# Kernel tuning notes

Measured on AMD Instinct MI355X. Metric: run time of the kernel, lower is better.

Reference implementation:

```python
import jax, jax.numpy as jnp
import numpy as np

B, T, D, H = 2, 2048, 1024, 16
Dh = D // H
SIG_SCALE = 1.0


def setup_inputs() -> dict:
    key = jax.random.key(0)
    ks = jax.random.split(key, 6)
    s = 1.0 / np.sqrt(D)
    return {
        "x": jax.random.normal(ks[0], (B, T, D), jnp.float32),
        "Wq": jax.random.normal(ks[1], (D, D), jnp.float32) * s,
        "Wk": jax.random.normal(ks[2], (D, D), jnp.float32) * s,
        "Wv": jax.random.normal(ks[3], (D, D), jnp.float32) * s,
        "Wb": jax.random.normal(ks[4], (D, H), jnp.float32) * s,
        "o_gamma": jnp.ones((H, Dh), jnp.float32),
        "Wo": jax.random.normal(ks[5], (D, D), jnp.float32) * s,
        "ln_g": jnp.ones((D,), jnp.float32),
        "ln_b": jnp.zeros((D,), jnp.float32),
    }


def _l2norm(a):
    return a * jax.lax.rsqrt(jnp.sum(a * a, -1, keepdims=True) + 1e-6)


def _deltanet(x, Wq, Wk, Wv, Wb, o_gamma, Wo):
    # bf16 projections (Block casts input to bfloat16), fp32 recurrence
    xb = x.astype(jnp.bfloat16)
    q = (xb @ Wq.astype(jnp.bfloat16)).astype(jnp.float32).reshape(B, T, H, Dh)
    k = (xb @ Wk.astype(jnp.bfloat16)).astype(jnp.float32).reshape(B, T, H, Dh)
    v = (xb @ Wv.astype(jnp.bfloat16)).astype(jnp.float32).reshape(B, T, H, Dh)
    q = _l2norm(jax.nn.silu(q))
    k = _l2norm(jax.nn.silu(k))
    # beta in [0, 2]: allows negative eigenvalues of (I - beta k k^T)
    beta = 2.0 * SIG_SCALE * jax.nn.sigmoid(
        (xb @ Wb.astype(jnp.bfloat16)).astype(jnp.float32))  # (B,T,H)

    def tohead(a):  # (B,T,H,Dh) -> (B*H, T, Dh)
        return a.transpose(0, 2, 1, 3).reshape(B * H, T, Dh)

    qh, kh, vh = tohead(q), tohead(k), tohead(v)
    bh = beta.transpose(0, 2, 1).reshape(B * H, T)

    def scan_one(qs, ks, vs, bs):
        def step(S, inp):
            k_t, v_t, q_t, b_t = inp
            # delta rule: S <- S + beta * (v - S k) k^T
            S = S + b_t * jnp.outer(v_t - S @ k_t, k_t)
            return S, S @ q_t
        _, o = jax.lax.scan(step, jnp.zeros((Dh, Dh), jnp.float32),
                            (ks, vs, qs, bs))
        return o  # (T, Dh)

    o = jax.vmap(scan_one)(qh, kh, vh, bh)  # (B*H, T, Dh)
    o = o.reshape(B, H, T, Dh).transpose(0, 2, 1, 3)  # (B,T,H,Dh)
    # per-head RMSNorm then output projection
    o = o * jax.lax.rsqrt(jnp.mean(o * o, -1, keepdims=True) + 1e-6) * o_gamma
    o = (o.reshape(B, T, D).astype(jnp.bfloat16) @ Wo.astype(jnp.bfloat16))
    return o.astype(jnp.float32)


def reference(x, Wq, Wk, Wv, Wb, o_gamma, Wo, ln_g, ln_b):
    y = _deltanet(x, Wq, Wk, Wv, Wb, o_gamma, Wo) + x  # residual in fp32
    mu = jnp.mean(y, -1, keepdims=True)
    var = jnp.mean(jnp.square(y - mu), -1, keepdims=True)
    y = (y - mu) * jax.lax.rsqrt(var + 1e-5) * ln_g + ln_b
    return y  # dropout is identity at inference; v_first passthrough is None
```

## Files before the change

### kernel.cpp

```cpp
#include <hip/hip_runtime.h>
#include <hip/hip_bf16.h>
#include <cstdint>

#define BB 2
#define TT 2048
#define DD 1024
#define HH 16
#define DH 64
#define MM (BB*TT)
constexpr int KDIM = 1024;
constexpr int NDIM = 1024;

typedef __bf16 bf16;
typedef __attribute__((ext_vector_type(8))) __bf16 bf16x8;
typedef __attribute__((ext_vector_type(4))) float f32x4;

#define MFMA(a,b,c) __builtin_amdgcn_mfma_f32_16x16x32_bf16((a),(b),(c),0,0,0)

__global__ __launch_bounds__(256) void k_cvt(const float* __restrict__ in, bf16* __restrict__ outp) {
    size_t i = ((size_t)blockIdx.x * 256 + threadIdx.x) * 8;
    float4 a = *(const float4*)(in + i);
    float4 b = *(const float4*)(in + i + 4);
    bf16x8 r;
    r[0] = (bf16)a.x; r[1] = (bf16)a.y; r[2] = (bf16)a.z; r[3] = (bf16)a.w;
    r[4] = (bf16)b.x; r[5] = (bf16)b.y; r[6] = (bf16)b.z; r[7] = (bf16)b.w;
    *(bf16x8*)(outp + i) = r;
}

__global__ __launch_bounds__(256) void k_transpose_cvt(const float* __restrict__ in, bf16* __restrict__ outp) {
    __shared__ float tile[64][65];
    const int tx = threadIdx.x & 63;
    const int ty = threadIdx.x >> 6;
    const int r0 = blockIdx.y * 64, c0 = blockIdx.x * 64;
#pragma unroll
    for (int i = 0; i < 16; ++i) {
        int rr = ty * 16 + i;
        tile[rr][tx] = in[(size_t)(r0 + rr) * 1024 + c0 + tx];
    }
    __syncthreads();
#pragma unroll
    for (int i = 0; i < 16; ++i) {
        int rr = ty * 16 + i;
        outp[(size_t)(c0 + rr) * 1024 + r0 + tx] = (bf16)tile[tx][rr];
    }
}

#define BM 128
#define BN 128
#define BKT 64

__device__ __forceinline__ void gemm_core(const bf16* __restrict__ A, const bf16* __restrict__ Bt,
                                          float* __restrict__ Cc) {
    __shared__ __align__(16) bf16 As[BM * BKT];
    __shared__ __align__(16) bf16 Bs[BN * BKT];
    const int tid  = threadIdx.x;
    const int lane = tid & 63;
    const int w    = tid >> 6;
    const int wr   = w >> 1, wc = w & 1;
    const int bm   = blockIdx.x * BM;
    const int bn   = blockIdx.y * BN;

    f32x4 acc[4][4];
#pragma unroll
    for (int m_ = 0; m_ < 4; ++m_)
#pragma unroll
        for (int n = 0; n < 4; ++n) acc[m_][n] = (f32x4){0.f, 0.f, 0.f, 0.f};

    const int srow = tid >> 3;
    const int sc   = tid & 7;
    const int sp   = sc ^ (srow & 7);
    const int fr   = lane & 15;
    const int fg   = lane >> 4;

    const bf16* Ap = A  + (size_t)(bm + srow) * KDIM + sc * 8;
    const bf16* Bp = Bt + (size_t)(bn + srow) * KDIM + sc * 8;

    for (int kt = 0; kt < KDIM; kt += BKT) {
        bf16x8 ar[4], br[4];
#pragma unroll
        for (int i = 0; i < 4; ++i) {
            ar[i] = *(const bf16x8*)(Ap + (size_t)i * 32 * KDIM + kt);
            br[i] = *(const bf16x8*)(Bp + (size_t)i * 32 * KDIM + kt);
        }
// ... 123 lines not shown
        if (t + 1 < TT) {
            const float* kn = kp + (size_t)(t + 1) * DD;
            const float* qn = qp + (size_t)(t + 1) * DD;
            nk0 = *(const float4*)(kn + 0);  nk1 = *(const float4*)(kn + 4);
            nk2 = *(const float4*)(kn + 8);  nk3 = *(const float4*)(kn + 12);
            nq0 = *(const float4*)(qn + 0);  nq1 = *(const float4*)(qn + 4);
            nq2 = *(const float4*)(qn + 8);  nq3 = *(const float4*)(qn + 12);
            nvv = vp[(size_t)(t + 1) * DD];
            nbt = bp[(size_t)(t + 1) * HH];
        }
        float a0, a1, a2, a3;
        a0 = S[0] * k0.x;  a1 = S[1] * k0.y;  a2 = S[2] * k0.z;  a3 = S[3] * k0.w;
        a0 = fmaf(S[4],  k1.x, a0); a1 = fmaf(S[5],  k1.y, a1); a2 = fmaf(S[6],  k1.z, a2); a3 = fmaf(S[7],  k1.w, a3);
        a0 = fmaf(S[8],  k2.x, a0); a1 = fmaf(S[9],  k2.y, a1); a2 = fmaf(S[10], k2.z, a2); a3 = fmaf(S[11], k2.w, a3);
        a0 = fmaf(S[12], k3.x, a0); a1 = fmaf(S[13], k3.y, a1); a2 = fmaf(S[14], k3.z, a2); a3 = fmaf(S[15], k3.w, a3);
        float sk = (a0 + a1) + (a2 + a3);
        sk += __shfl_xor(sk, 1); sk += __shfl_xor(sk, 2);
        const float wgt = bt * (vv - sk);
        float o0, o1, o2, o3;
        S[0]  = fmaf(wgt, k0.x, S[0]);  o0 = S[0] * q0.x;
        S[1]  = fmaf(wgt, k0.y, S[1]);  o1 = S[1] * q0.y;
        S[2]  = fmaf(wgt, k0.z, S[2]);  o2 = S[2] * q0.z;
        S[3]  = fmaf(wgt, k0.w, S[3]);  o3 = S[3] * q0.w;
        S[4]  = fmaf(wgt, k1.x, S[4]);  o0 = fmaf(S[4],  q1.x, o0);
        S[5]  = fmaf(wgt, k1.y, S[5]);  o1 = fmaf(S[5],  q1.y, o1);
        S[6]  = fmaf(wgt, k1.z, S[6]);  o2 = fmaf(S[6],  q1.z, o2);
        S[7]  = fmaf(wgt, k1.w, S[7]);  o3 = fmaf(S[7],  q1.w, o3);
        S[8]  = fmaf(wgt, k2.x, S[8]);  o0 = fmaf(S[8],  q2.x, o0);
        S[9]  = fmaf(wgt, k2.y, S[9]);  o1 = fmaf(S[9],  q2.y, o1);
        S[10] = fmaf(wgt, k2.z, S[10]); o2 = fmaf(S[10], q2.z, o2);
        S[11] = fmaf(wgt, k2.w, S[11]); o3 = fmaf(S[11], q2.w, o3);
        S[12] = fmaf(wgt, k3.x, S[12]); o0 = fmaf(S[12], q3.x, o0);
        S[13] = fmaf(wgt, k3.y, S[13]); o1 = fmaf(S[13], q3.y, o1);
        S[14] = fmaf(wgt, k3.z, S[14]); o2 = fmaf(S[14], q3.z, o2);
        S[15] = fmaf(wgt, k3.w, S[15]); o3 = fmaf(S[15], q3.w, o3);
        float oo = (o0 + o1) + (o2 + o3);
        oo += __shfl_xor(oo, 1); oo += __shfl_xor(oo, 2);
        if (seg == 0) op[(size_t)t * DD] = oo;
        k0 = nk0; k1 = nk1; k2 = nk2; k3 = nk3;
        q0 = nq0; q1 = nq1; q2 = nq2; q3 = nq3;
        vv = nvv; bt = nbt;
    }
}


__device__ __forceinline__ int uv_idx(int t, int vv) {
    return (((t >> 4) * 4 + (vv >> 4)) * 64 + (((t >> 2) & 3) * 16 + (vv & 15))) * 4 + (t & 3);
}

__global__ __launch_bounds__(256, 3) void k_prep(
        const float* __restrict__ q, const float* __restrict__ k, const float* __restrict__ v,
        const float* __restrict__ beta,
        bf16* __restrict__ L_out, bf16* __restrict__ nUk_h, bf16* __restrict__ nUk_l,
        bf16* __restrict__ Kt_h, bf16* __restrict__ Kt_l, float* __restrict__ Uv_out) {
    __shared__ float Ash[64][65];
    __shared__ bf16 Khi[64][72], Klo[64][72];
    __shared__ float bsh[64];

    const int tid = threadIdx.x;
    const int c = blockIdx.x, bh = blockIdx.y, b = bh >> 4, h = bh & 15;
    const int row0 = b * TT + c * 64, col0 = h * 64;
    const size_t off = ((size_t)bh * 32 + c) * 4096;
    const int lane = tid & 63, w = tid >> 6;
    const int fr = lane & 15, fg = lane >> 4;

    const int cslice = (w & 1) * 32;
    const float* rp = ((w >= 2) ? k : v) + (size_t)(row0 + lane) * DD + col0 + cslice;
    float4 rv[8];
#pragma unroll
    for (int a = 0; a < 8; ++a) rv[a] = *(const float4*)(rp + a * 4);
    const float* qfp = q + (size_t)(row0 + w * 16 + fr) * DD + col0 + fg * 8;
    float4 qa = *(const float4*)qfp, qb = *(const float4*)(qfp + 4);
    float4 qc = *(const float4*)(qfp + 32), qd = *(const float4*)(qfp + 36);
    const int tr = tid >> 2, cs = (tid & 3) * 16;
    float4 kv[4];
    const size_t rb = (size_t)(row0 + tr) * DD + col0 + cs;
#pragma unroll
    for (int j = 0; j < 4; ++j) kv[j] = *(const float4*)(k + rb + j * 4);

    if (tid < 64) bsh[tid] = beta[(size_t)(row0 + tid) * HH + h];
#pragma unroll
    for (int j = 0; j < 4; ++j) {
        int cb = cs + j * 4;
        float a0 = kv[j].x, a1 = kv[j].y, a2 = kv[j].z, a3 = kv[j].w;
        bf16 h0 = (bf16)a0, h1 = (bf16)a1, h2 = (bf16)a2, h3 = (bf16)a3;
        Khi[tr][cb] = h0; Khi[tr][cb+1] = h1; Khi[tr][cb+2] = h2; Khi[tr][cb+3] = h3;
        Klo[tr][cb]   = (bf16)(a0 - (float)h0);
        Klo[tr][cb+1] = (bf16)(a1 - (float)h1);
        Klo[tr][cb+2] = (bf16)(a2 - (float)h2);
        Klo[tr][cb+3] = (bf16)(a3 - (float)h3);
    }
    __syncthreads();

    {
        bf16x8 aqh0, aqh1;
        aqh0[0]=(bf16)qa.x; aqh0[1]=(bf16)qa.y; aqh0[2]=(bf16)qa.z; aqh0[3]=(bf16)qa.w;
        aqh0[4]=(bf16)qb.x; aqh0[5]=(bf16)qb.y; aqh0[6]=(bf16)qb.z; aqh0[7]=(bf16)qb.w;
        aqh1[0]=(bf16)qc.x; aqh1[1]=(bf16)qc.y; aqh1[2]=(bf16)qc.z; aqh1[3]=(bf16)qc.w;
        aqh1[4]=(bf16)qd.x; aqh1[5]=(bf16)qd.y; aqh1[6]=(bf16)qd.z; aqh1[7]=(bf16)qd.w;
        f32x4 accA[4], accL[4];
#pragma unroll
        for (int it = 0; it < 4; ++it) { accA[it] = (f32x4){0,0,0,0}; accL[it] = (f32x4){0,0,0,0}; }
        bf16x8 akh0 = *(const bf16x8*)&Khi[w*16+fr][fg*8];
        bf16x8 akh1 = *(const bf16x8*)&Khi[w*16+fr][fg*8+32];
        bf16x8 akl0 = *(const bf16x8*)&Klo[w*16+fr][fg*8];
        bf16x8 akl1 = *(const bf16x8*)&Klo[w*16+fr][fg*8+32];
#pragma unroll
        for (int it = 0; it < 4; ++it) {
            bf16x8 bh0 = *(const bf16x8*)&Khi[it*16+fr][fg*8];
            bf16x8 bl0 = *(const bf16x8*)&Klo[it*16+fr][fg*8];
            accA[it] = MFMA(akh0, bh0, accA[it]);
            accA[it] = MFMA(akh0, bl0, accA[it]);
            accA[it] = MFMA(akl0, bh0, accA[it]);
            accL[it] = MFMA(aqh0, bh0, accL[it]);
            bf16x8 bh1 = *(const bf16x8*)&Khi[it*16+fr][fg*8+32];
            bf16x8 bl1 = *(const bf16x8*)&Klo[it*16+fr][fg*8+32];
            accA[it] = MFMA(akh1, bh1, accA[it]);
            accA[it] = MFMA(akh1, bl1, accA[it]);
            accA[it] = MFMA(akl1, bh1, accA[it]);
            accL[it] = MFMA(aqh1, bh1, accL[it]);
        }
#pragma unroll
        for (int it = 0; it < 4; ++it)
#pragma unroll
            for (int j = 0; j < 4; ++j) {
                int tg = w * 16 + fg * 4 + j, ig = it * 16 + fr;
                Ash[tg][ig] = (ig < tg) ? bsh[tg] * accA[it][j] : 0.f;
                L_out[off + tg * 64 + ig] = (ig <= tg) ? (bf16)accL[it][j] : (bf16)0.f;
            }
    }
    __syncthreads();

    float bt = bsh[lane];
    float X[32];
#pragma unroll
    for (int a = 0; a < 8; ++a) {
        X[a*4+0] = bt * rv[a].x; X[a*4+1] = bt * rv[a].y;
        X[a*4+2] = bt * rv[a].z; X[a*4+3] = bt * rv[a].w;
    }
#pragma unroll 1
    for (int i = 0; i < 63; ++i) {
        float a = Ash[lane][i];
#pragma unroll
        for (int j = 0; j < 32; ++j) {
            float s = __uint_as_float(__builtin_amdgcn_readlane(__float_as_uint(X[j]), i));
            X[j] = fmaf(-a, s, X[j]);
        }
    }

    if (w < 2) {
#pragma unroll
        for (int j = 0; j < 32; ++j)
            Uv_out[off + uv_idx(lane, cslice + j)] = X[j];
    } else {
#pragma unroll
        for (int g = 0; g < 4; ++g) {
            bf16x8 hi8, lo8;
#pragma unroll
            for (int e = 0; e < 8; ++e) {
                float nk = -X[g*8+e];
                bf16 nh = (bf16)nk;
                hi8[e] = nh;
                lo8[e] = (bf16)(nk - (float)nh);
            }
            *(bf16x8*)(nUk_h + off + (size_t)lane*64 + cslice + g*8) = hi8;
            *(bf16x8*)(nUk_l + off + (size_t)lane*64 + cslice + g*8) = lo8;
        }
    }
#pragma unroll
    for (int j = 0; j < 16; ++j) {
        int vc = cs + j;
        Kt_h[off + (size_t)tr*64 + vc] = Khi[vc][tr];
        Kt_l[off + (size_t)tr*64 + vc] = Klo[vc][tr];
    }
}

struct Frag {
    bf16x8 nkh0, nkh1, nkl0, nkl1;
    bf16x8 kth0, kth1, ktl0, ktl1;
    bf16x8 lf0, lf1;
    float4 qa, qb, qc, qd;
    f32x4 uv0, uv1, uv2, uv3;
};

__device__ __forceinline__ void load_frags(Frag& F,
        const bf16* __restrict__ nUk_h, const bf16* __restrict__ nUk_l,
        const bf16* __restrict__ Kt_h, const bf16* __restrict__ Kt_l,
        const bf16* __restrict__ L_in, const float* __restrict__ Uv_in,
        const float* __restrict__ q, size_t off, size_t qbase, int w, int lane) {
    const int fr = lane & 15, fg = lane >> 4;
    const size_t ra = off + (size_t)(w * 16 + fr) * 64 + fg * 8;
    F.nkh0 = *(const bf16x8*)(nUk_h + ra); F.nkh1 = *(const bf16x8*)(nUk_h + ra + 32);
    F.nkl0 = *(const bf16x8*)(nUk_l + ra); F.nkl1 = *(const bf16x8*)(nUk_l + ra + 32);
    F.kth0 = *(const bf16x8*)(Kt_h + ra);  F.kth1 = *(const bf16x8*)(Kt_h + ra + 32);
    F.ktl0 = *(const bf16x8*)(Kt_l + ra);  F.ktl1 = *(const bf16x8*)(Kt_l + ra + 32);
    F.lf0  = *(const bf16x8*)(L_in + ra);  F.lf1  = *(const bf16x8*)(L_in + ra + 32);
    const float* qp = q + qbase + (size_t)(w * 16 + fr) * DD + fg * 8;
    F.qa = *(const float4*)qp;        F.qb = *(const float4*)(qp + 4);
    F.qc = *(const float4*)(qp + 32); F.qd = *(const float4*)(qp + 36);
    const float* up = Uv_in + off + w * 1024 + lane * 4;
    F.uv0 = *(const f32x4*)up;         F.uv1 = *(const f32x4*)(up + 256);
    F.uv2 = *(const f32x4*)(up + 512); F.uv3 = *(const f32x4*)(up + 768);
}

__device__ __forceinline__ void compute_chunk(const Frag& F, f32x4 (&Sacc)[4],
        float* __restrict__ o, int row0c, int col0, int w, int lane,
        bf16 (*ShT_h)[72], bf16 (*ShT_l)[72], bf16 (*Ut_h)[72], bf16 (*Ut_l)[72]) {
    const int fr = lane & 15, fg = lane >> 4;
    f32x4 Uacc[4] = {F.uv0, F.uv1, F.uv2, F.uv3};
#pragma unroll
    for (int vt = 0; vt < 4; ++vt) {
        const bf16* sh0 = &ShT_h[vt * 16 + fr][fg * 8];
        const bf16* sl0 = &ShT_l[vt * 16 + fr][fg * 8];
        bf16x8 sh = *(const bf16x8*)sh0, sl = *(const bf16x8*)sl0;
        Uacc[vt] = MFMA(F.nkh0, sh, Uacc[vt]);
        Uacc[vt] = MFMA(F.nkh0, sl, Uacc[vt]);
        Uacc[vt] = MFMA(F.nkl0, sh, Uacc[vt]);
        sh = *(const bf16x8*)(sh0 + 32); sl = *(const bf16x8*)(sl0 + 32);
        Uacc[vt] = MFMA(F.nkh1, sh, Uacc[vt]);
        Uacc[vt] = MFMA(F.nkh1, sl, Uacc[vt]);
        Uacc[vt] = MFMA(F.nkl1, sh, Uacc[vt]);
    }
#pragma unroll
    for (int vt = 0; vt < 4; ++vt) {
        int vg = vt * 16 + fr;
#pragma unroll
        for (int j = 0; j < 4; ++j) {
            int tg = w * 16 + fg * 4 + j;
            float u = Uacc[vt][j];
            bf16 hh = (bf16)u;
            Ut_h[vg][tg] = hh;
            Ut_l[vg][tg] = (bf16)(u - (float)hh);
        }
    }
    __syncthreads();
    bf16x8 q0, q1;
    q0[0]=(bf16)F.qa.x; q0[1]=(bf16)F.qa.y; q0[2]=(bf16)F.qa.z; q0[3]=(bf16)F.qa.w;
    q0[4]=(bf16)F.qb.x; q0[5]=(bf16)F.qb.y; q0[6]=(bf16)F.qb.z; q0[7]=(bf16)F.qb.w;
    q1[0]=(bf16)F.qc.x; q1[1]=(bf16)F.qc.y; q1[2]=(bf16)F.qc.z; q1[3]=(bf16)F.qc.w;
    q1[4]=(bf16)F.qd.x; q1[5]=(bf16)F.qd.y; q1[6]=(bf16)F.qd.z; q1[7]=(bf16)F.qd.w;
    f32x4 Oacc[4];
#pragma unroll
    for (int vt = 0; vt < 4; ++vt) Oacc[vt] = (f32x4){0, 0, 0, 0};
#pragma unroll
    for (int vt = 0; vt < 4; ++vt) {
        const bf16* uh0 = &Ut_h[vt * 16 + fr][fg * 8];
        const bf16* ul0 = &Ut_l[vt * 16 + fr][fg * 8];
        const bf16* so0 = &ShT_h[vt * 16 + fr][fg * 8];
        bf16x8 uh = *(const bf16x8*)uh0, ul = *(const bf16x8*)ul0, so = *(const bf16x8*)so0;
        Sacc[vt] = MFMA(F.kth0, uh, Sacc[vt]);
        Sacc[vt] = MFMA(F.kth0, ul, Sacc[vt]);
        Sacc[vt] = MFMA(F.ktl0, uh, Sacc[vt]);
        Oacc[vt] = MFMA(q0, so, Oacc[vt]);
        Oacc[vt] = MFMA(F.lf0, uh, Oacc[vt]);
        uh = *(const bf16x8*)(uh0 + 32); ul = *(const bf16x8*)(ul0 + 32); so = *(const bf16x8*)(so0 + 32);
        Sacc[vt] = MFMA(F.kth1, uh, Sacc[vt]);
        Sacc[vt] = MFMA(F.kth1, ul, Sacc[vt]);
        Sacc[vt] = MFMA(F.ktl1, uh, Sacc[vt]);
        Oacc[vt] = MFMA(q1, so, Oacc[vt]);
        Oacc[vt] = MFMA(F.lf1, uh, Oacc[vt]);
    }
    __syncthreads();
#pragma unroll
    for (int vt = 0; vt < 4; ++vt) {
        int vg = vt * 16 + fr;
#pragma unroll
        for (int j = 0; j < 4; ++j) {
            int tg = w * 16 + fg * 4 + j;
            o[(size_t)(row0c + tg) * DD + col0 + vg] = Oacc[vt][j];
            float s = Sacc[vt][j];
            bf16 hh = (bf16)s;
            ShT_h[vg][tg] = hh;
            ShT_l[vg][tg] = (bf16)(s - (float)hh);
        }
    }
    __syncthreads();
}

__global__ __launch_bounds__(256, 1) void k_scan2(
        const float* __restrict__ q, const bf16* __restrict__ L_in,
        const bf16* __restrict__ nUk_h, const bf16* __restrict__ nUk_l,
        const bf16* __restrict__ Kt_h, const bf16* __restrict__ Kt_l,
        const float* __restrict__ Uv_in, float* __restrict__ o) {
    __shared__ bf16 ShT_h[64][72], ShT_l[64][72], Ut_h[64][72], Ut_l[64][72];
    const int tid = threadIdx.x, lane = tid & 63, w = tid >> 6;
    const int bh = blockIdx.x, b = bh >> 4, hh = bh & 15;
    const int col0 = hh * 64;
    for (int i = tid; i < 64 * 72; i += 256) {
        (&ShT_h[0][0])[i] = (bf16)0.f;
        (&ShT_l[0][0])[i] = (bf16)0.f;
    }
    __syncthreads();
    f32x4 Sacc[4];
#pragma unroll
    for (int vt = 0; vt < 4; ++vt) Sacc[vt] = (f32x4){0, 0, 0, 0};

    Frag fA, fB;
    auto offc = [&](int c) { return ((size_t)bh * 32 + c) * 4096; };
    auto qbasec = [&](int c) { return (size_t)(b * TT + c * 64) * DD + col0; };
    load_frags(fA, nUk_h, nUk_l, Kt_h, Kt_l, L_in, Uv_in, q, offc(0), qbasec(0), w, lane);
    for (int c = 0; c < 32; c += 2) {
        load_frags(fB, nUk_h, nUk_l, Kt_h, Kt_l, L_in, Uv_in, q, offc(c + 1), qbasec(c + 1), w, lane);
        compute_chunk(fA, Sacc, o, b * TT + c * 64, col0, w, lane, ShT_h, ShT_l, Ut_h, Ut_l);
        if (c + 2 < 32)
            load_frags(fA, nUk_h, nUk_l, Kt_h, Kt_l, L_in, Uv_in, q, offc(c + 2), qbasec(c + 2), w, lane);
        compute_chunk(fB, Sacc, o, b * TT + (c + 1) * 64, col0, w, lane, ShT_h, ShT_l, Ut_h, Ut_l);
    }
}

__global__ __launch_bounds__(256) void k_rms(const float* __restrict__ o, const float* __restrict__ gm,
                                             bf16* __restrict__ obf) {
    size_t row = (size_t)blockIdx.x * 4 + (threadIdx.x >> 6);
    int lane = threadIdx.x & 63;
    int h = (int)(row & 15);
    float x = o[row * 64 + lane];
    float ss = x * x;
#pragma unroll
    for (int m = 1; m < 64; m <<= 1) ss += __shfl_xor(ss, m);
    float y = x * rsqrtf(ss * (1.f / 64.f) + 1e-6f) * gm[h * 64 + lane];
    obf[row * 64 + lane] = (bf16)y;
}

__global__ __launch_bounds__(256) void k_ln(const float* __restrict__ yp, const float* __restrict__ x,
                                            const float* __restrict__ g, const float* __restrict__ bb,
                                            float* __restrict__ outp) {
    const int row = blockIdx.x;
    const int tid = threadIdx.x;
    __shared__ float red[8];
    const size_t base = (size_t)row * DD + tid * 4;
    float4 a  = *(const float4*)(yp + base);
    float4 b4 = *(const float4*)(x + base);
    float y0 = a.x + b4.x, y1 = a.y + b4.y, y2 = a.z + b4.z, y3 = a.w + b4.w;
    float s = (y0 + y1) + (y2 + y3);
#pragma unroll
    for (int m = 1; m < 64; m <<= 1) s += __shfl_xor(s, m);
    if ((tid & 63) == 0) red[tid >> 6] = s;
    __syncthreads();
    float mu = (red[0] + red[1] + red[2] + red[3]) * (1.f / (float)DD);
    float d0 = y0 - mu, d1 = y1 - mu, d2 = y2 - mu, d3 = y3 - mu;
    float sq = (d0 * d0 + d1 * d1) + (d2 * d2 + d3 * d3);
#pragma unroll
    for (int m = 1; m < 64; m <<= 1) sq += __shfl_xor(sq, m);
    if ((tid & 63) == 0) red[4 + (tid >> 6)] = sq;
    __syncthreads();
    float var = (red[4] + red[5] + red[6] + red[7]) * (1.f / (float)DD);
    float inv = rsqrtf(var + 1e-5f);
    const int c = tid * 4;
    float4 gg = *(const float4*)(g + c);
    float4 bv = *(const float4*)(bb + c);
    float4 r;
    r.x = d0 * inv * gg.x + bv.x;
    r.y = d1 * inv * gg.y + bv.y;
    r.z = d2 * inv * gg.z + bv.z;
    r.w = d3 * inv * gg.w + bv.w;
    *(float4*)(outp + base) = r;
}

extern "C" void kernel_launch(void* const* d_in, const int* in_sizes, int n_in,
                              void* d_out, int out_size, void* d_ws, size_t ws_size,
                              hipStream_t stream) {
    (void)in_sizes; (void)n_in; (void)out_size;
    if (ws_size < ((size_t)81 << 20)) return;
    const bool fast = ws_size >= ((size_t)137 << 20);

    const float* x   = (const float*)d_in[0];
    const float* Wq  = (const float*)d_in[1];
    const float* Wk  = (const float*)d_in[2];
    const float* Wv  = (const float*)d_in[3];
    const float* Wb  = (const float*)d_in[4];
    const float* gma = (const float*)d_in[5];
    const float* Wo  = (const float*)d_in[6];
    const float* lng = (const float*)d_in[7];
    const float* lnb = (const float*)d_in[8];
    float* outp = (float*)d_out;

    char* ws = (char*)d_ws;
    bf16*  xb    = (bf16*)(ws);
    bf16*  WqT   = (bf16*)(ws + ((size_t)8  << 20));
    bf16*  WoT   = (bf16*)(ws + ((size_t)14 << 20));
    float* q     = (float*)(ws + ((size_t)16 << 20));
    float* k     = (float*)(ws + ((size_t)32 << 20));
    float* v     = (float*)(ws + ((size_t)48 << 20));
    float* beta  = (float*)(ws + ((size_t)64 << 20));
    bf16*  wf    = (bf16*)(ws + ((size_t)64 << 20) + (1 << 19));
    float* o     = (float*)(ws + ((size_t)65 << 20));
    bf16*  obf   = (bf16*)(ws);
    float* yproj = (float*)(ws + ((size_t)16 << 20));
    bf16*  Lbf   = (bf16*)(ws + ((size_t)81  << 20));
    bf16*  nUk_h = (bf16*)(ws + ((size_t)89  << 20));
    bf16*  nUk_l = (bf16*)(ws + ((size_t)97  << 20));
    bf16*  Kt_h  = (bf16*)(ws + ((size_t)105 << 20));
    bf16*  Kt_l  = (bf16*)(ws + ((size_t)113 << 20));
    float* Uv    = (float*)(ws + ((size_t)121 << 20));

    bf16* WkT = WqT + (size_t)DD * DD;
    bf16* WvT = WkT + (size_t)DD * DD;

    k_wbfrag<<<8, 256, 0, stream>>>(Wb, wf);
    k_cvt<<<2048, 256, 0, stream>>>(x, xb);
    dim3 tg(16, 16);
    k_transpose_cvt<<<tg, 256, 0, stream>>>(Wq, WqT);
    k_transpose_cvt<<<tg, 256, 0, stream>>>(Wk, WkT);
    k_transpose_cvt<<<tg, 256, 0, stream>>>(Wv, WvT);
    k_transpose_cvt<<<tg, 256, 0, stream>>>(Wo, WoT);
    k_gemm_qkv<<<dim3(32, 8, 3), 256, 0, stream>>>(xb, WqT, q);
    k_beta2<<<256, 64, 0, stream>>>(xb, wf, beta);
    k_actnorm<<<16384, 256, 0, stream>>>(q);
    k_actnorm<<<16384, 256, 0, stream>>>(k);
    if (fast) {
        k_prep<<<dim3(32, 32), 256, 0, stream>>>(q, k, v, beta, Lbf, nUk_h, nUk_l, Kt_h, Kt_l, Uv);
        k_scan2<<<32, 256, 0, stream>>>(q, Lbf, nUk_h, nUk_l, Kt_h, Kt_l, Uv, o);
    } else {
        k_scan<<<32, 256, 0, stream>>>(q, k, v, beta, o);
    }
    k_rms<<<16384, 256, 0, stream>>>(o, gma, obf);
    k_gemm<<<dim3(32, 8), 256, 0, stream>>>(obf, WoT, yproj);
    k_ln<<<4096, 256, 0, stream>>>(yproj, x, lng, lnb, outp);
}
```

Before: 342.1 us.

## Warp-specialize chunked scan: state waves and output waves overlap across chunks

The chunked delta-rule scan kernel now launches 512 threads. Four waves run the serial state recurrence (U and S updates), while four other waves compute the output for the previous chunk from double-buffered shared-memory copies of S and U. This takes the output MFMAs and q loading off the serial critical path. Output is written in a fragment-native chunk layout, and a new RMS-norm kernel reads that layout and scatters bf16 results in row-major order. The cost is doubled shared memory, a scattered write pattern in the norm kernel, and an extra pipeline stage to drain at the end.

```diff
diff --git a/kernel.cpp b/kernel.cpp
--- a/kernel.cpp
+++ b/kernel.cpp
@@ -381,136 +381,174 @@
     }
 }
 
-struct Frag {
-    bf16x8 nkh0, nkh1, nkl0, nkl1;
-    bf16x8 kth0, kth1, ktl0, ktl1;
-    bf16x8 lf0, lf1;
-    float4 qa, qb, qc, qd;
-    f32x4 uv0, uv1, uv2, uv3;
-};
-
-__device__ __forceinline__ void load_frags(Frag& F,
-        const bf16* __restrict__ nUk_h, const bf16* __restrict__ nUk_l,
-        const bf16* __restrict__ Kt_h, const bf16* __restrict__ Kt_l,
-        const bf16* __restrict__ L_in, const float* __restrict__ Uv_in,
-        const float* __restrict__ q, size_t off, size_t qbase, int w, int lane) {
-    const int fr = lane & 15, fg = lane >> 4;
-    const size_t ra = off + (size_t)(w * 16 + fr) * 64 + fg * 8;
-    F.nkh0 = *(const bf16x8*)(nUk_h + ra); F.nkh1 = *(const bf16x8*)(nUk_h + ra + 32);
-    F.nkl0 = *(const bf16x8*)(nUk_l + ra); F.nkl1 = *(const bf16x8*)(nUk_l + ra + 32);
-    F.kth0 = *(const bf16x8*)(Kt_h + ra);  F.kth1 = *(const bf16x8*)(Kt_h + ra + 32);
-    F.ktl0 = *(const bf16x8*)(Kt_l + ra);  F.ktl1 = *(const bf16x8*)(Kt_l + ra + 32);
-    F.lf0  = *(const bf16x8*)(L_in + ra);  F.lf1  = *(const bf16x8*)(L_in + ra + 32);
-    const float* qp = q + qbase + (size_t)(w * 16 + fr) * DD + fg * 8;
-    F.qa = *(const float4*)qp;        F.qb = *(const float4*)(qp + 4);
-    F.qc = *(const float4*)(qp + 32); F.qd = *(const float4*)(qp + 36);
-    const float* up = Uv_in + off + w * 1024 + lane * 4;
-    F.uv0 = *(const f32x4*)up;         F.uv1 = *(const f32x4*)(up + 256);
-    F.uv2 = *(const f32x4*)(up + 512); F.uv3 = *(const f32x4*)(up + 768);
-}
-
-__device__ __forceinline__ void compute_chunk(const Frag& F, f32x4 (&Sacc)[4],
-        float* __restrict__ o, int row0c, int col0, int w, int lane,
-        bf16 (*ShT_h)[72], bf16 (*ShT_l)[72], bf16 (*Ut_h)[72], bf16 (*Ut_l)[72]) {
-    const int fr = lane & 15, fg = lane >> 4;
-    f32x4 Uacc[4] = {F.uv0, F.uv1, F.uv2, F.uv3};
-#pragma unroll
-    for (int vt = 0; vt < 4; ++vt) {
-        const bf16* sh0 = &ShT_h[vt * 16 + fr][fg * 8];
-        const bf16* sl0 = &ShT_l[vt * 16 + fr][fg * 8];
-        bf16x8 sh = *(const bf16x8*)sh0, sl = *(const bf16x8*)sl0;
-        Uacc[vt] = MFMA(F.nkh0, sh, Uacc[vt]);
-        Uacc[vt] = MFMA(F.nkh0, sl, Uacc[vt]);
-        Uacc[vt] = MFMA(F.nkl0, sh, Uacc[vt]);
-        sh = *(const bf16x8*)(sh0 + 32); sl = *(const bf16x8*)(sl0 + 32);
-        Uacc[vt] = MFMA(F.nkh1, sh, Uacc[vt]);
-        Uacc[vt] = MFMA(F.nkh1, sl, Uacc[vt]);
-        Uacc[vt] = MFMA(F.nkl1, sh, Uacc[vt]);
-    }
-#pragma unroll
-    for (int vt = 0; vt < 4; ++vt) {
-        int vg = vt * 16 + fr;
-#pragma unroll
-        for (int j = 0; j < 4; ++j) {
-            int tg = w * 16 + fg * 4 + j;
-            float u = Uacc[vt][j];
-            bf16 hh = (bf16)u;
-            Ut_h[vg][tg] = hh;
-            Ut_l[vg][tg] = (bf16)(u - (float)hh);
-        }
-    }
-    __syncthreads();
-    bf16x8 q0, q1;
-    q0[0]=(bf16)F.qa.x; q0[1]=(bf16)F.qa.y; q0[2]=(bf16)F.qa.z; q0[3]=(bf16)F.qa.w;
-    q0[4]=(bf16)F.qb.x; q0[5]=(bf16)F.qb.y; q0[6]=(bf16)F.qb.z; q0[7]=(bf16)F.qb.w;
-    q1[0]=(bf16)F.qc.x; q1[1]=(bf16)F.qc.y; q1[2]=(bf16)F.qc.z; q1[3]=(bf16)F.qc.w;
-    q1[4]=(bf16)F.qd.x; q1[5]=(bf16)F.qd.y; q1[6]=(bf16)F.qd.z; q1[7]=(bf16)F.qd.w;
-    f32x4 Oacc[4];
-#pragma unroll
-    for (int vt = 0; vt < 4; ++vt) Oacc[vt] = (f32x4){0, 0, 0, 0};
-#pragma unroll
-    for (int vt = 0; vt < 4; ++vt) {
-        const bf16* uh0 = &Ut_h[vt * 16 + fr][fg * 8];
-        const bf16* ul0 = &Ut_l[vt * 16 + fr][fg * 8];
-        const bf16* so0 = &ShT_h[vt * 16 + fr][fg * 8];
-        bf16x8 uh = *(const bf16x8*)uh0, ul = *(const bf16x8*)ul0, so = *(const bf16x8*)so0;
-        Sacc[vt] = MFMA(F.kth0, uh, Sacc[vt]);
-        Sacc[vt] = MFMA(F.kth0, ul, Sacc[vt]);
-        Sacc[vt] = MFMA(F.ktl0, uh, Sacc[vt]);
-        Oacc[vt] = MFMA(q0, so, Oacc[vt]);
-        Oacc[vt] = MFMA(F.lf0, uh, Oacc[vt]);
-        uh = *(const bf16x8*)(uh0 + 32); ul = *(const bf16x8*)(ul0 + 32); so = *(const bf16x8*)(so0 + 32);
-        Sacc[vt] = MFMA(F.kth1, uh, Sacc[vt]);
-        Sacc[vt] = MFMA(F.kth1, ul, Sacc[vt]);
-        Sacc[vt] = MFMA(F.ktl1, uh, Sacc[vt]);
-        Oacc[vt] = MFMA(q1, so, Oacc[vt]);
-        Oacc[vt] = MFMA(F.lf1, uh, Oacc[vt]);
-    }
-    __syncthreads();
-#pragma unroll
-    for (int vt = 0; vt < 4; ++vt) {
-        int vg = vt * 16 + fr;
-#pragma unroll
-        for (int j = 0; j < 4; ++j) {
-            int tg = w * 16 + fg * 4 + j;
-            o[(size_t)(row0c + tg) * DD + col0 + vg] = Oacc[vt][j];
-            float s = Sacc[vt][j];
-            bf16 hh = (bf16)s;
-            ShT_h[vg][tg] = hh;
-            ShT_l[vg][tg] = (bf16)(s - (float)hh);
-        }
-    }
-    __syncthreads();
-}
-
-__global__ __launch_bounds__(256, 1) void k_scan2(
+__global__ __launch_bounds__(512, 2) void k_scan2(
         const float* __restrict__ q, const bf16* __restrict__ L_in,
         const bf16* __restrict__ nUk_h, const bf16* __restrict__ nUk_l,
         const bf16* __restrict__ Kt_h, const bf16* __restrict__ Kt_l,
-        const float* __restrict__ Uv_in, float* __restrict__ o) {
-    __shared__ bf16 ShT_h[64][72], ShT_l[64][72], Ut_h[64][72], Ut_l[64][72];
-    const int tid = threadIdx.x, lane = tid & 63, w = tid >> 6;
+        const float* __restrict__ Uv_in, float* __restrict__ of) {
+    __shared__ bf16 ShT_h[2][64][72], ShT_l[2][64][72], Ut_h[2][64][72], Ut_l[2][64][72];
+    const int tid = threadIdx.x, lane = tid & 63, wid = tid >> 6;
+    const int w = wid & 3;
+    const bool SR = (wid < 4);
     const int bh = blockIdx.x, b = bh >> 4, hh = bh & 15;
     const int col0 = hh * 64;
-    for (int i = tid; i < 64 * 72; i += 256) {
-        (&ShT_h[0][0])[i] = (bf16)0.f;
-        (&ShT_l[0][0])[i] = (bf16)0.f;
+    const int fr = lane & 15, fg = lane >> 4;
+
+    {
+        bf16* z0 = &ShT_h[0][0][0]; bf16* z1 = &ShT_l[0][0][0];
+        for (int i = tid; i < 64 * 72; i += 512) { z0[i] = (bf16)0.f; z1[i] = (bf16)0.f; }
     }
     __syncthreads();
+
+    auto offc = [&](int c) { return ((size_t)bh * 32 + c) * 4096; };
+    auto rac  = [&](int c) { return offc(c) + (size_t)(w * 16 + fr) * 64 + fg * 8; };
+
     f32x4 Sacc[4];
-#pragma unroll
-    for (int vt = 0; vt < 4; ++vt) Sacc[vt] = (f32x4){0, 0, 0, 0};
-
-    Frag fA, fB;
-    auto offc = [&](int c) { return ((size_t)bh * 32 + c) * 4096; };
-    auto qbasec = [&](int c) { return (size_t)(b * TT + c * 64) * DD + col0; };
-    load_frags(fA, nUk_h, nUk_l, Kt_h, Kt_l, L_in, Uv_in, q, offc(0), qbasec(0), w, lane);
-    for (int c = 0; c < 32; c += 2) {
-        load_frags(fB, nUk_h, nUk_l, Kt_h, Kt_l, L_in, Uv_in, q, offc(c + 1), qbasec(c + 1), w, lane);
-        compute_chunk(fA, Sacc, o, b * TT + c * 64, col0, w, lane, ShT_h, ShT_l, Ut_h, Ut_l);
-        if (c + 2 < 32)
-            load_frags(fA, nUk_h, nUk_l, Kt_h, Kt_l, L_in, Uv_in, q, offc(c + 2), qbasec(c + 2), w, lane);
-        compute_chunk(fB, Sacc, o, b * TT + (c + 1) * 64, col0, w, lane, ShT_h, ShT_l, Ut_h, Ut_l);
+    bf16x8 nkh0, nkh1, nkl0, nkl1, kth0, kth1, ktl0, ktl1;
+    f32x4 uv0, uv1, uv2, uv3;
+    bf16x8 lf0, lf1, qf0, qf1;
+
+    if (SR) {
+#pragma unroll
+        for (int vt = 0; vt < 4; ++vt) Sacc[vt] = (f32x4){0, 0, 0, 0};
+        size_t ra = rac(0);
+        nkh0 = *(const bf16x8*)(nUk_h + ra); nkh1 = *(const bf16x8*)(nUk_h + ra + 32);
+        nkl0 = *(const bf16x8*)(nUk_l + ra); nkl1 = *(const bf16x8*)(nUk_l + ra + 32);
+        kth0 = *(const bf16x8*)(Kt_h + ra);  kth1 = *(const bf16x8*)(Kt_h + ra + 32);
+        ktl0 = *(const bf16x8*)(Kt_l + ra);  ktl1 = *(const bf16x8*)(Kt_l + ra + 32);
+        const float* up = Uv_in + offc(0) + w * 1024 + lane * 4;
+        uv0 = *(const f32x4*)up;         uv1 = *(const f32x4*)(up + 256);
+        uv2 = *(const f32x4*)(up + 512); uv3 = *(const f32x4*)(up + 768);
+    }
+
+    for (int c = 0; c < 32; ++c) {
+        const int p = c & 1;
+        bf16x8 tnkh0, tnkh1, tnkl0, tnkl1, tkth0, tkth1, tktl0, tktl1;
+        f32x4 tuv0, tuv1, tuv2, tuv3;
+        bf16x8 tlf0, tlf1, tqf0, tqf1;
+
+        if (SR) {
+            if (c < 31) {
+                size_t ra = rac(c + 1);
+                tnkh0 = *(const bf16x8*)(nUk_h + ra); tnkh1 = *(const bf16x8*)(nUk_h + ra + 32);
+                tnkl0 = *(const bf16x8*)(nUk_l + ra); tnkl1 = *(const bf16x8*)(nUk_l + ra + 32);
+                tkth0 = *(const bf16x8*)(Kt_h + ra);  tkth1 = *(const bf16x8*)(Kt_h + ra + 32);
+                tktl0 = *(const bf16x8*)(Kt_l + ra);  tktl1 = *(const bf16x8*)(Kt_l + ra + 32);
+                const float* up = Uv_in + offc(c + 1) + w * 1024 + lane * 4;
+                tuv0 = *(const f32x4*)up;         tuv1 = *(const f32x4*)(up + 256);
+                tuv2 = *(const f32x4*)(up + 512); tuv3 = *(const f32x4*)(up + 768);
+            }
+            f32x4 Uacc[4] = {uv0, uv1, uv2, uv3};
+#pragma unroll
+            for (int vt = 0; vt < 4; ++vt) {
+                const bf16* sh0 = &ShT_h[p][vt * 16 + fr][fg * 8];
+                const bf16* sl0 = &ShT_l[p][vt * 16 + fr][fg * 8];
+                bf16x8 sh = *(const bf16x8*)sh0, sl = *(const bf16x8*)sl0;
+                Uacc[vt] = MFMA(nkh0, sh, Uacc[vt]);
+                Uacc[vt] = MFMA(nkh0, sl, Uacc[vt]);
+                Uacc[vt] = MFMA(nkl0, sh, Uacc[vt]);
+                sh = *(const bf16x8*)(sh0 + 32); sl = *(const bf16x8*)(sl0 + 32);
+                Uacc[vt] = MFMA(nkh1, sh, Uacc[vt]);
+                Uacc[vt] = MFMA(nkh1, sl, Uacc[vt]);
+                Uacc[vt] = MFMA(nkl1, sh, Uacc[vt]);
+            }
+#pragma unroll
+            for (int vt = 0; vt < 4; ++vt) {
+                int vg = vt * 16 + fr;
+#pragma unroll
+                for (int j = 0; j < 4; ++j) {
+                    int tg = w * 16 + fg * 4 + j;
+                    float u = Uacc[vt][j];
+                    bf16 hhv = (bf16)u;
+                    Ut_h[p][vg][tg] = hhv;
+                    Ut_l[p][vg][tg] = (bf16)(u - (float)hhv);
+                }
+            }
+        } else {
+            size_t ra = rac(c);
+            tlf0 = *(const bf16x8*)(L_in + ra); tlf1 = *(const bf16x8*)(L_in + ra + 32);
+            const float* qp = q + (size_t)(b * TT + c * 64 + w * 16 + fr) * DD + col0 + fg * 8;
+            float4 qa = *(const float4*)qp,        qb = *(const float4*)(qp + 4);
+            float4 qc = *(const float4*)(qp + 32), qd = *(const float4*)(qp + 36);
+            tqf0[0]=(bf16)qa.x; tqf0[1]=(bf16)qa.y; tqf0[2]=(bf16)qa.z; tqf0[3]=(bf16)qa.w;
+            tqf0[4]=(bf16)qb.x; tqf0[5]=(bf16)qb.y; tqf0[6]=(bf16)qb.z; tqf0[7]=(bf16)qb.w;
+            tqf1[0]=(bf16)qc.x; tqf1[1]=(bf16)qc.y; tqf1[2]=(bf16)qc.z; tqf1[3]=(bf16)qc.w;
+            tqf1[4]=(bf16)qd.x; tqf1[5]=(bf16)qd.y; tqf1[6]=(bf16)qd.z; tqf1[7]=(bf16)qd.w;
+            if (c > 0) {
+                f32x4 Oacc[4];
+#pragma unroll
+                for (int vt = 0; vt < 4; ++vt) Oacc[vt] = (f32x4){0, 0, 0, 0};
+#pragma unroll
+                for (int vt = 0; vt < 4; ++vt) {
+                    const bf16* so0 = &ShT_h[1 - p][vt * 16 + fr][fg * 8];
+                    const bf16* uh0 = &Ut_h[1 - p][vt * 16 + fr][fg * 8];
+                    bf16x8 so = *(const bf16x8*)so0, uh = *(const bf16x8*)uh0;
+                    Oacc[vt] = MFMA(qf0, so, Oacc[vt]);
+                    Oacc[vt] = MFMA(lf0, uh, Oacc[vt]);
+                    so = *(const bf16x8*)(so0 + 32); uh = *(const bf16x8*)(uh0 + 32);
+                    Oacc[vt] = MFMA(qf1, so, Oacc[vt]);
+                    Oacc[vt] = MFMA(lf1, uh, Oacc[vt]);
+                }
+                float* ob = of + offc(c - 1) + (size_t)(w * 4) * 256 + (size_t)lane * 4;
+#pragma unroll
+                for (int vt = 0; vt < 4; ++vt) *(f32x4*)(ob + vt * 256) = Oacc[vt];
+            }
+        }
+        __syncthreads();
+        if (SR) {
+#pragma unroll
+            for (int vt = 0; vt < 4; ++vt) {
+                const bf16* uh0 = &Ut_h[p][vt * 16 + fr][fg * 8];
+                const bf16* ul0 = &Ut_l[p][vt * 16 + fr][fg * 8];
+                bf16x8 uh = *(const bf16x8*)uh0, ul = *(const bf16x8*)ul0;
+                Sacc[vt] = MFMA(kth0, uh, Sacc[vt]);
+                Sacc[vt] = MFMA(kth0, ul, Sacc[vt]);
+                Sacc[vt] = MFMA(ktl0, uh, Sacc[vt]);
+                uh = *(const bf16x8*)(uh0 + 32); ul = *(const bf16x8*)(ul0 + 32);
+                Sacc[vt] = MFMA(kth1, uh, Sacc[vt]);
+                Sacc[vt] = MFMA(kth1, ul, Sacc[vt]);
+                Sacc[vt] = MFMA(ktl1, uh, Sacc[vt]);
+            }
+            if (c < 31) {
+#pragma unroll
+                for (int vt = 0; vt < 4; ++vt) {
+                    int vg = vt * 16 + fr;
+#pragma unroll
+                    for (int j = 0; j < 4; ++j) {
+                        int tg = w * 16 + fg * 4 + j;
+                        float s = Sacc[vt][j];
+                        bf16 hhv = (bf16)s;
+                        ShT_h[1 - p][vg][tg] = hhv;
+                        ShT_l[1 - p][vg][tg] = (bf16)(s - (float)hhv);
+                    }
+                }
+                nkh0 = tnkh0; nkh1 = tnkh1; nkl0 = tnkl0; nkl1 = tnkl1;
+                kth0 = tkth0; kth1 = tkth1; ktl0 = tktl0; ktl1 = tktl1;
+                uv0 = tuv0; uv1 = tuv1; uv2 = tuv2; uv3 = tuv3;
+            }
+        } else {
+            lf0 = tlf0; lf1 = tlf1; qf0 = tqf0; qf1 = tqf1;
+        }
+        __syncthreads();
+    }
+    if (!SR) {
+        f32x4 Oacc[4];
+#pragma unroll
+        for (int vt = 0; vt < 4; ++vt) Oacc[vt] = (f32x4){0, 0, 0, 0};
+#pragma unroll
+        for (int vt = 0; vt < 4; ++vt) {
+            const bf16* so0 = &ShT_h[1][vt * 16 + fr][fg * 8];
+            const bf16* uh0 = &Ut_h[1][vt * 16 + fr][fg * 8];
+            bf16x8 so = *(const bf16x8*)so0, uh = *(const bf16x8*)uh0;
+            Oacc[vt] = MFMA(qf0, so, Oacc[vt]);
+            Oacc[vt] = MFMA(lf0, uh, Oacc[vt]);
+            so = *(const bf16x8*)(so0 + 32); uh = *(const bf16x8*)(uh0 + 32);
+            Oacc[vt] = MFMA(qf1, so, Oacc[vt]);
+            Oacc[vt] = MFMA(lf1, uh, Oacc[vt]);
+        }
+        float* ob = of + offc(31) + (size_t)(w * 4) * 256 + (size_t)lane * 4;
+#pragma unroll
+        for (int vt = 0; vt < 4; ++vt) *(f32x4*)(ob + vt * 256) = Oacc[vt];
     }
 }
 
@@ -525,6 +563,45 @@
     for (int m = 1; m < 64; m <<= 1) ss += __shfl_xor(ss, m);
     float y = x * rsqrtf(ss * (1.f / 64.f) + 1e-6f) * gm[h * 64 + lane];
     obf[row * 64 + lane] = (bf16)y;
+}
+
+__global__ __launch_bounds__(256) void k_rms2(const float* __restrict__ of, const float* __restrict__ gm,
+                                              bf16* __restrict__ obf) {
+    const int c = blockIdx.x, bh = blockIdx.y;
+    const int b = bh >> 4, h = bh & 15;
+    const int tid = threadIdx.x, lane = tid & 63, w = tid >> 6;
+    const int fr = lane & 15, fg = lane >> 4;
+    const size_t off = ((size_t)bh * 32 + c) * 4096;
+    f32x4 val[4];
+    float ss0 = 0.f, ss1 = 0.f, ss2 = 0.f, ss3 = 0.f;
+#pragma unroll
+    for (int vt = 0; vt < 4; ++vt) {
+        val[vt] = *(const f32x4*)(of + off + (size_t)((w * 4 + vt) * 64 + lane) * 4);
+        ss0 += val[vt][0] * val[vt][0];
+        ss1 += val[vt][1] * val[vt][1];
+        ss2 += val[vt][2] * val[vt][2];
+        ss3 += val[vt][3] * val[vt][3];
+    }
+#pragma unroll
+    for (int m = 1; m < 16; m <<= 1) {
+        ss0 += __shfl_xor(ss0, m); ss1 += __shfl_xor(ss1, m);
+        ss2 += __shfl_xor(ss2, m); ss3 += __shfl_xor(ss3, m);
+    }
+    float r0 = rsqrtf(ss0 * (1.f / 64.f) + 1e-6f);
+    float r1 = rsqrtf(ss1 * (1.f / 64.f) + 1e-6f);
+    float r2 = rsqrtf(ss2 * (1.f / 64.f) + 1e-6f);
+    float r3 = rsqrtf(ss3 * (1.f / 64.f) + 1e-6f);
+    const int row0 = b * TT + c * 64 + w * 16 + fg * 4;
+#pragma unroll
+    for (int vt = 0; vt < 4; ++vt) {
+        int vg = vt * 16 + fr;
+        float g = gm[h * 64 + vg];
+        size_t base = (size_t)row0 * DD + h * 64 + vg;
+        obf[base]          = (bf16)(val[vt][0] * r0 * g);
+        obf[base + DD]     = (bf16)(val[vt][1] * r1 * g);
+        obf[base + 2 * DD] = (bf16)(val[vt][2] * r2 * g);
+        obf[base + 3 * DD] = (bf16)(val[vt][3] * r3 * g);
+    }
 }
 
 __global__ __launch_bounds__(256) void k_ln(const float* __restrict__ yp, const float* __restrict__ x,
@@ -615,11 +692,12 @@
     k_actnorm<<<16384, 256, 0, stream>>>(k);
     if (fast) {
         k_prep<<<dim3(32, 32), 256, 0, stream>>>(q, k, v, beta, Lbf, nUk_h, nUk_l, Kt_h, Kt_l, Uv);
-        k_scan2<<<32, 256, 0, stream>>>(q, Lbf, nUk_h, nUk_l, Kt_h, Kt_l, Uv, o);
+        k_scan2<<<32, 512, 0, stream>>>(q, Lbf, nUk_h, nUk_l, Kt_h, Kt_l, Uv, o);
+        k_rms2<<<dim3(32, 32), 256, 0, stream>>>(o, gma, obf);
     } else {
         k_scan<<<32, 256, 0, stream>>>(q, k, v, beta, o);
-    }
-    k_rms<<<16384, 256, 0, stream>>>(o, gma, obf);
+        k_rms<<<16384, 256, 0, stream>>>(o, gma, obf);
+    }
     k_gemm<<<dim3(32, 8), 256, 0, stream>>>(obf, WoT, yproj);
     k_ln<<<4096, 256, 0, stream>>>(yproj, x, lng, lnb, outp);
 }
```

Result: no change. 346.9 us (+1.4%).

## Fuse RMSNorm into scan, prepack bf16 Q fragments, merge transposes and actnorm launches

Applied to the files above, without the earlier changes.

The per-head RMSNorm and bf16 cast are now done inside the chunked scan kernel, using shuffle reductions across the MFMA output fragment and writing bf16 directly. This removes the fp32 o round trip and the separate k_rms launch. The prep kernel also writes Q as prepacked bf16 fragments, so the serial scan loads half the bytes and skips the conversions. The four weight transposes are merged into one launch, and the q/k actnorm runs as a single doubled-grid launch, which assumes k sits contiguously after q.

```diff
diff --git a/kernel.cpp b/kernel.cpp
--- a/kernel.cpp
+++ b/kernel.cpp
@@ -27,8 +27,19 @@
     *(bf16x8*)(outp + i) = r;
 }
 
-__global__ __launch_bounds__(256) void k_transpose_cvt(const float* __restrict__ in, bf16* __restrict__ outp) {
+__global__ __launch_bounds__(256) void k_transpose_cvt4(
+        const float* __restrict__ i0, const float* __restrict__ i1,
+        const float* __restrict__ i2, const float* __restrict__ i3,
+        bf16* __restrict__ o0, bf16* __restrict__ o1,
+        bf16* __restrict__ o2, bf16* __restrict__ o3) {
     __shared__ float tile[64][65];
+    const float* in; bf16* outp;
+    switch (blockIdx.z) {
+        case 0:  in = i0; outp = o0; break;
+        case 1:  in = i1; outp = o1; break;
+        case 2:  in = i2; outp = o2; break;
+        default: in = i3; outp = o3; break;
+    }
     const int tx = threadIdx.x & 63;
     const int ty = threadIdx.x >> 6;
     const int r0 = blockIdx.y * 64, c0 = blockIdx.x * 64;
@@ -258,7 +269,8 @@
         const float* __restrict__ q, const float* __restrict__ k, const float* __restrict__ v,
         const float* __restrict__ beta,
         bf16* __restrict__ L_out, bf16* __restrict__ nUk_h, bf16* __restrict__ nUk_l,
-        bf16* __restrict__ Kt_h, bf16* __restrict__ Kt_l, float* __restrict__ Uv_out) {
+        bf16* __restrict__ Kt_h, bf16* __restrict__ Kt_l, float* __restrict__ Uv_out,
+        bf16* __restrict__ Qf) {
     __shared__ float Ash[64][65];
     __shared__ bf16 Khi[64][72], Klo[64][72];
     __shared__ float bsh[64];
@@ -304,6 +316,11 @@
         aqh0[4]=(bf16)qb.x; aqh0[5]=(bf16)qb.y; aqh0[6]=(bf16)qb.z; aqh0[7]=(bf16)qb.w;
         aqh1[0]=(bf16)qc.x; aqh1[1]=(bf16)qc.y; aqh1[2]=(bf16)qc.z; aqh1[3]=(bf16)qc.w;
         aqh1[4]=(bf16)qd.x; aqh1[5]=(bf16)qd.y; aqh1[6]=(bf16)qd.z; aqh1[7]=(bf16)qd.w;
+        {
+            const size_t ra = off + (size_t)(w * 16 + fr) * 64 + fg * 8;
+            *(bf16x8*)(Qf + ra) = aqh0;
+            *(bf16x8*)(Qf + ra + 32) = aqh1;
+        }
         f32x4 accA[4], accL[4];
 #pragma unroll
         for (int it = 0; it < 4; ++it) { accA[it] = (f32x4){0,0,0,0}; accL[it] = (f32x4){0,0,0,0}; }
@@ -384,16 +401,15 @@
 struct Frag {
     bf16x8 nkh0, nkh1, nkl0, nkl1;
     bf16x8 kth0, kth1, ktl0, ktl1;
-    bf16x8 lf0, lf1;
-    float4 qa, qb, qc, qd;
+    bf16x8 lf0, lf1, qf0, qf1;
     f32x4 uv0, uv1, uv2, uv3;
 };
 
 __device__ __forceinline__ void load_frags(Frag& F,
         const bf16* __restrict__ nUk_h, const bf16* __restrict__ nUk_l,
         const bf16* __restrict__ Kt_h, const bf16* __restrict__ Kt_l,
-        const bf16* __restrict__ L_in, const float* __restrict__ Uv_in,
-        const float* __restrict__ q, size_t off, size_t qbase, int w, int lane) {
+        const bf16* __restrict__ L_in, const bf16* __restrict__ Qf,
+        const float* __restrict__ Uv_in, size_t off, int w, int lane) {
     const int fr = lane & 15, fg = lane >> 4;
     const size_t ra = off + (size_t)(w * 16 + fr) * 64 + fg * 8;
     F.nkh0 = *(const bf16x8*)(nUk_h + ra); F.nkh1 = *(const bf16x8*)(nUk_h + ra + 32);
@@ -401,16 +417,14 @@
     F.kth0 = *(const bf16x8*)(Kt_h + ra);  F.kth1 = *(const bf16x8*)(Kt_h + ra + 32);
     F.ktl0 = *(const bf16x8*)(Kt_l + ra);  F.ktl1 = *(const bf16x8*)(Kt_l + ra + 32);
     F.lf0  = *(const bf16x8*)(L_in + ra);  F.lf1  = *(const bf16x8*)(L_in + ra + 32);
-    const float* qp = q + qbase + (size_t)(w * 16 + fr) * DD + fg * 8;
-    F.qa = *(const float4*)qp;        F.qb = *(const float4*)(qp + 4);
-    F.qc = *(const float4*)(qp + 32); F.qd = *(const float4*)(qp + 36);
+    F.qf0  = *(const bf16x8*)(Qf + ra);    F.qf1  = *(const bf16x8*)(Qf + ra + 32);
     const float* up = Uv_in + off + w * 1024 + lane * 4;
     F.uv0 = *(const f32x4*)up;         F.uv1 = *(const f32x4*)(up + 256);
     F.uv2 = *(const f32x4*)(up + 512); F.uv3 = *(const f32x4*)(up + 768);
 }
 
 __device__ __forceinline__ void compute_chunk(const Frag& F, f32x4 (&Sacc)[4],
-        float* __restrict__ o, int row0c, int col0, int w, int lane,
+        bf16* __restrict__ obf, const float (&gmv)[4], int row0c, int col0, int w, int lane,
         bf16 (*ShT_h)[72], bf16 (*ShT_l)[72], bf16 (*Ut_h)[72], bf16 (*Ut_l)[72]) {
     const int fr = lane & 15, fg = lane >> 4;
     f32x4 Uacc[4] = {F.uv0, F.uv1, F.uv2, F.uv3};
@@ -440,11 +454,6 @@
         }
     }
     __syncthreads();
-    bf16x8 q0, q1;
-    q0[0]=(bf16)F.qa.x; q0[1]=(bf16)F.qa.y; q0[2]=(bf16)F.qa.z; q0[3]=(bf16)F.qa.w;
-    q0[4]=(bf16)F.qb.x; q0[5]=(bf16)F.qb.y; q0[6]=(bf16)F.qb.z; q0[7]=(bf16)F.qb.w;
-    q1[0]=(bf16)F.qc.x; q1[1]=(bf16)F.qc.y; q1[2]=(bf16)F.qc.z; q1[3]=(bf16)F.qc.w;
-    q1[4]=(bf16)F.qd.x; q1[5]=(bf16)F.qd.y; q1[6]=(bf16)F.qd.z; q1[7]=(bf16)F.qd.w;
     f32x4 Oacc[4];
 #pragma unroll
     for (int vt = 0; vt < 4; ++vt) Oacc[vt] = (f32x4){0, 0, 0, 0};
@@ -457,37 +466,60 @@
         Sacc[vt] = MFMA(F.kth0, uh, Sacc[vt]);
         Sacc[vt] = MFMA(F.kth0, ul, Sacc[vt]);
         Sacc[vt] = MFMA(F.ktl0, uh, Sacc[vt]);
-        Oacc[vt] = MFMA(q0, so, Oacc[vt]);
+        Oacc[vt] = MFMA(F.qf0, so, Oacc[vt]);
         Oacc[vt] = MFMA(F.lf0, uh, Oacc[vt]);
         uh = *(const bf16x8*)(uh0 + 32); ul = *(const bf16x8*)(ul0 + 32); so = *(const bf16x8*)(so0 + 32);
         Sacc[vt] = MFMA(F.kth1, uh, Sacc[vt]);
         Sacc[vt] = MFMA(F.kth1, ul, Sacc[vt]);
         Sacc[vt] = MFMA(F.ktl1, uh, Sacc[vt]);
-        Oacc[vt] = MFMA(q1, so, Oacc[vt]);
+        Oacc[vt] = MFMA(F.qf1, so, Oacc[vt]);
         Oacc[vt] = MFMA(F.lf1, uh, Oacc[vt]);
     }
     __syncthreads();
+    float ss0 = 0.f, ss1 = 0.f, ss2 = 0.f, ss3 = 0.f;
+#pragma unroll
+    for (int vt = 0; vt < 4; ++vt) {
+        ss0 += Oacc[vt][0] * Oacc[vt][0];
+        ss1 += Oacc[vt][1] * Oacc[vt][1];
+        ss2 += Oacc[vt][2] * Oacc[vt][2];
+        ss3 += Oacc[vt][3] * Oacc[vt][3];
+    }
+#pragma unroll
+    for (int m = 1; m < 16; m <<= 1) {
+        ss0 += __shfl_xor(ss0, m); ss1 += __shfl_xor(ss1, m);
+        ss2 += __shfl_xor(ss2, m); ss3 += __shfl_xor(ss3, m);
+    }
+    float r0 = rsqrtf(ss0 * (1.f / 64.f) + 1e-6f);
+    float r1 = rsqrtf(ss1 * (1.f / 64.f) + 1e-6f);
+    float r2 = rsqrtf(ss2 * (1.f / 64.f) + 1e-6f);
+    float r3 = rsqrtf(ss3 * (1.f / 64.f) + 1e-6f);
+    const size_t orow = (size_t)(row0c + w * 16 + fg * 4) * DD + col0;
 #pragma unroll
     for (int vt = 0; vt < 4; ++vt) {
         int vg = vt * 16 + fr;
 #pragma unroll
         for (int j = 0; j < 4; ++j) {
             int tg = w * 16 + fg * 4 + j;
-            o[(size_t)(row0c + tg) * DD + col0 + vg] = Oacc[vt][j];
             float s = Sacc[vt][j];
             bf16 hh = (bf16)s;
             ShT_h[vg][tg] = hh;
             ShT_l[vg][tg] = (bf16)(s - (float)hh);
         }
+        float g = gmv[vt];
+        obf[orow + vg]          = (bf16)(Oacc[vt][0] * r0 * g);
+        obf[orow + DD + vg]     = (bf16)(Oacc[vt][1] * r1 * g);
+        obf[orow + 2 * DD + vg] = (bf16)(Oacc[vt][2] * r2 * g);
+        obf[orow + 3 * DD + vg] = (bf16)(Oacc[vt][3] * r3 * g);
     }
     __syncthreads();
 }
 
 __global__ __launch_bounds__(256, 1) void k_scan2(
-        const float* __restrict__ q, const bf16* __restrict__ L_in,
+        const bf16* __restrict__ Qf, const bf16* __restrict__ L_in,
         const bf16* __restrict__ nUk_h, const bf16* __restrict__ nUk_l,
         const bf16* __restrict__ Kt_h, const bf16* __restrict__ Kt_l,
-        const float* __restrict__ Uv_in, float* __restrict__ o) {
+        const float* __restrict__ Uv_in, const float* __restrict__ gm,
+        bf16* __restrict__ obf) {
     __shared__ bf16 ShT_h[64][72], ShT_l[64][72], Ut_h[64][72], Ut_l[64][72];
     const int tid = threadIdx.x, lane = tid & 63, w = tid >> 6;
     const int bh = blockIdx.x, b = bh >> 4, hh = bh & 15;
@@ -500,17 +532,19 @@
     f32x4 Sacc[4];
 #pragma unroll
     for (int vt = 0; vt < 4; ++vt) Sacc[vt] = (f32x4){0, 0, 0, 0};
+    float gmv[4];
+#pragma unroll
+    for (int vt = 0; vt < 4; ++vt) gmv[vt] = gm[hh * 64 + vt * 16 + (lane & 15)];
 
     Frag fA, fB;
     auto offc = [&](int c) { return ((size_t)bh * 32 + c) * 4096; };
-    auto qbasec = [&](int c) { return (size_t)(b * TT + c * 64) * DD + col0; };
-    load_frags(fA, nUk_h, nUk_l, Kt_h, Kt_l, L_in, Uv_in, q, offc(0), qbasec(0), w, lane);
+    load_frags(fA, nUk_h, nUk_l, Kt_h, Kt_l, L_in, Qf, Uv_in, offc(0), w, lane);
     for (int c = 0; c < 32; c += 2) {
-        load_frags(fB, nUk_h, nUk_l, Kt_h, Kt_l, L_in, Uv_in, q, offc(c + 1), qbasec(c + 1), w, lane);
-        compute_chunk(fA, Sacc, o, b * TT + c * 64, col0, w, lane, ShT_h, ShT_l, Ut_h, Ut_l);
+        load_frags(fB, nUk_h, nUk_l, Kt_h, Kt_l, L_in, Qf, Uv_in, offc(c + 1), w, lane);
+        compute_chunk(fA, Sacc, obf, gmv, b * TT + c * 64, col0, w, lane, ShT_h, ShT_l, Ut_h, Ut_l);
         if (c + 2 < 32)
-            load_frags(fA, nUk_h, nUk_l, Kt_h, Kt_l, L_in, Uv_in, q, offc(c + 2), qbasec(c + 2), w, lane);
-        compute_chunk(fB, Sacc, o, b * TT + (c + 1) * 64, col0, w, lane, ShT_h, ShT_l, Ut_h, Ut_l);
+            load_frags(fA, nUk_h, nUk_l, Kt_h, Kt_l, L_in, Qf, Uv_in, offc(c + 2), w, lane);
+        compute_chunk(fB, Sacc, obf, gmv, b * TT + (c + 1) * 64, col0, w, lane, ShT_h, ShT_l, Ut_h, Ut_l);
     }
 }
 
@@ -590,6 +624,7 @@
     float* beta  = (float*)(ws + ((size_t)64 << 20));
     bf16*  wf    = (bf16*)(ws + ((size_t)64 << 20) + (1 << 19));
     float* o     = (float*)(ws + ((size_t)65 << 20));
+    bf16*  Qfrag = (bf16*)(ws + ((size_t)65 << 20));
     bf16*  obf   = (bf16*)(ws);
     float* yproj = (float*)(ws + ((size_t)16 << 20));
     bf16*  Lbf   = (bf16*)(ws + ((size_t)81  << 20));
@@ -604,22 +639,17 @@
 
     k_wbfrag<<<8, 256, 0, stream>>>(Wb, wf);
     k_cvt<<<2048, 256, 0, stream>>>(x, xb);
-    dim3 tg(16, 16);
-    k_transpose_cvt<<<tg, 256, 0, stream>>>(Wq, WqT);
-    k_transpose_cvt<<<tg, 256, 0, stream>>>(Wk, WkT);
-    k_transpose_cvt<<<tg, 256, 0, stream>>>(Wv, WvT);
-    k_transpose_cvt<<<tg, 256, 0, stream>>>(Wo, WoT);
+    k_transpose_cvt4<<<dim3(16, 16, 4), 256, 0, stream>>>(Wq, Wk, Wv, Wo, WqT, WkT, WvT, WoT);
     k_gemm_qkv<<<dim3(32, 8, 3), 256, 0, stream>>>(xb, WqT, q);
     k_beta2<<<256, 64, 0, stream>>>(xb, wf, beta);
-    k_actnorm<<<16384, 256, 0, stream>>>(q);
-    k_actnorm<<<16384, 256, 0, stream>>>(k);
+    k_actnorm<<<32768, 256, 0, stream>>>(q);
     if (fast) {
-        k_prep<<<dim3(32, 32), 256, 0, stream>>>(q, k, v, beta, Lbf, nUk_h, nUk_l, Kt_h, Kt_l, Uv);
-        k_scan2<<<32, 256, 0, stream>>>(q, Lbf, nUk_h, nUk_l, Kt_h, Kt_l, Uv, o);
+        k_prep<<<dim3(32, 32), 256, 0, stream>>>(q, k, v, beta, Lbf, nUk_h, nUk_l, Kt_h, Kt_l, Uv, Qfrag);
+        k_scan2<<<32, 256, 0, stream>>>(Qfrag, Lbf, nUk_h, nUk_l, Kt_h, Kt_l, Uv, gma, obf);
     } else {
         k_scan<<<32, 256, 0, stream>>>(q, k, v, beta, o);
-    }
-    k_rms<<<16384, 256, 0, stream>>>(o, gma, obf);
+        k_rms<<<16384, 256, 0, stream>>>(o, gma, obf);
+    }
     k_gemm<<<dim3(32, 8), 256, 0, stream>>>(obf, WoT, yproj);
     k_ln<<<4096, 256, 0, stream>>>(yproj, x, lng, lnb, outp);
 }
```

Result: faster. 326.9 us (-4.4%).
